# Kernel optimization log

Measured on AMD Instinct MI355X. Metric: run time of the kernel, lower is better.

## Reference

```python
import jax, jax.numpy as jnp
import numpy as np

B, C, H, W = 16, 128, 64, 64
NH = 8
HD = C // NH          # head dim == pos_embed_dim
WIN = 5               # relative-position window
OUT = 512             # out_dim of the final 1x1 projection


def _dwconv(x, w, pad):
    """Depthwise 2D conv, x: (N, Cin, H, W), w: (Cin, 1, kh, kw)."""
    return jax.lax.conv_general_dilated(
        x, w, window_strides=(1, 1), padding=[(pad, pad), (pad, pad)],
        dimension_numbers=('NCHW', 'OIHW', 'NCHW'),
        feature_group_count=x.shape[1])


def setup_inputs() -> dict:
    key = jax.random.key(0)
    ks = jax.random.split(key, 6)
    src = jax.random.normal(ks[0], (B, C, H, W), jnp.float32)
    cpe_w = jax.random.normal(ks[1], (C, 1, 3, 3), jnp.float32) * 0.1
    qkv_w = jax.random.normal(ks[2], (3 * C, C), jnp.float32) * (1.0 / np.sqrt(C))
    rel_pos = jax.random.normal(ks[3], (HD, WIN, WIN), jnp.float32) * 0.02
    conv1d_w = jax.random.normal(ks[4], (3,), jnp.float32) * 0.5
    out_w = jax.random.normal(ks[5], (OUT, 2 * C), jnp.float32) * (1.0 / np.sqrt(2 * C))
    return dict(src=src, cpe_w=cpe_w, qkv_w=qkv_w, rel_pos=rel_pos,
                conv1d_w=conv1d_w, out_w=out_w)


def reference(src, cpe_w, qkv_w, rel_pos, conv1d_w, out_w):
    scaling = HD ** (-0.5)
    feature_raw = src

    # CPE: depthwise 3x3 conv residual
    s = _dwconv(src, cpe_w, 1) + src

    # 1x1 QKV conv == channel GEMM
    qkv = jnp.einsum('oc,bchw->bohw', qkv_w, s)          # (B, 3C, H, W)
    q, k, v = jnp.split(qkv, 3, axis=1)                  # each (B, C, H, W)

    q = q.reshape(B * NH, HD, H, W)
    k = k.reshape(B * NH, HD, H, W)
    v = v.reshape(B * NH, HD, H, W)

    N = H * W
    kf = jax.nn.softmax(k.reshape(B * NH, HD, N), axis=-1)   # softmax over spatial
    vf = v.reshape(B * NH, HD, N)
    content_lambda = jnp.einsum('bin,bon->bio', kf, vf)      # (B*NH, HD, HD)
    qf = q.reshape(B * NH, HD, N) * scaling
    content_output = jnp.einsum('bin,bio->bon', qf, content_lambda)
    content_output = content_output.reshape(B * NH, HD, H, W)

    # relative-position lambda: depthwise 5x5 conv of v with rel_pos_embed
    position_lambda = _dwconv(v, rel_pos[:, None, :, :], WIN // 2)
    position_output = q * position_lambda

    result1 = (content_output + position_output).reshape(B, C, H, W)

    # ECA-style channel attention on the raw input
    pool = jnp.mean(feature_raw, axis=(2, 3))                # (B, C)
    xp = jnp.pad(pool, ((0, 0), (1, 1)))
    ca = jax.nn.sigmoid(conv1d_w[0] * xp[:, :-2]
                        + conv1d_w[1] * xp[:, 1:-1]
                        + conv1d_w[2] * xp[:, 2:])           # (B, C)
    result2 = feature_raw * ca[:, :, None, None]

    cat = jnp.concatenate([result1, result2], axis=1)       # (B, 2C, H, W)
    return jnp.einsum('oc,bchw->bohw', out_w, cat)           # (B, OUT, H, W)
```

## Files before the change

### kernel.cpp

```cpp
#include <hip/hip_runtime.h>
#include <hip/hip_bf16.h>
#include <math.h>

#define Bb   16
#define Cc   128
#define Hh   64
#define Wwid 64
#define Nn   4096
#define NHh  8
#define HDd  16
#define BHh  128
#define TCc  384
#define OUTc 512
#define KK2  256

typedef _Float16 f16x8 __attribute__((ext_vector_type(8)));
typedef float    f32x4 __attribute__((ext_vector_type(4)));

__device__ __forceinline__ ushort f2h_bits(float f) {
    _Float16 h = (_Float16)f;
    ushort u;
    __builtin_memcpy(&u, &h, 2);
    return u;
}
__device__ __forceinline__ float h2f_bits(ushort u) {
    _Float16 h;
    __builtin_memcpy(&h, &u, 2);
    return (float)h;
}

__global__ void __launch_bounds__(256) cpe_cvt_kernel(
        const float* __restrict__ src, const float* __restrict__ cpe_w,
        const float* __restrict__ qkv_w, const float* __restrict__ out_w,
        ushort* __restrict__ s, ushort* __restrict__ src16,
        float* __restrict__ pool,
        ushort* __restrict__ wq16, ushort* __restrict__ wo16) {
    int t = threadIdx.x;
    if (blockIdx.x >= 2048) {
        int i = (blockIdx.x - 2048) * 256 + t;
        const int na = TCc * Cc, nb = OUTc * KK2;
        if (i < na) wq16[i] = f2h_bits(qkv_w[i]);
        else if (i < na + nb) wo16[i - na] = f2h_bits(out_w[i - na]);
        return;
    }
    int bc = blockIdx.x;
    int c  = bc & (Cc - 1);
    const float* sp = src + (size_t)bc * Nn;
    __shared__ float pl[66 * 66];
    __shared__ float red[256];
    for (int i = t; i < 66 * 66; i += 256) pl[i] = 0.f;
    __syncthreads();
    float lsum = 0.f;
    ushort* s16p = src16 + (size_t)bc * Nn;
    for (int i = t; i < Nn / 4; i += 256) {
        float4 v4 = ((const float4*)sp)[i];
        lsum += v4.x + v4.y + v4.z + v4.w;
        ushort4 h4 = make_ushort4(f2h_bits(v4.x), f2h_bits(v4.y),
                                  f2h_bits(v4.z), f2h_bits(v4.w));
        *(ushort4*)(s16p + i * 4) = h4;
        int e = i * 4, y = e >> 6, x = e & 63;
        float* d = &pl[(y + 1) * 66 + x + 1];
        d[0] = v4.x; d[1] = v4.y; d[2] = v4.z; d[3] = v4.w;
    }
    red[t] = lsum;
    float w[9];
#pragma unroll
    for (int k = 0; k < 9; k++) w[k] = cpe_w[c * 9 + k];
    __syncthreads();
    for (int s2 = 128; s2 > 0; s2 >>= 1) {
        if (t < s2) red[t] += red[t + s2];
        __syncthreads();
    }
    if (t == 0) pool[bc] = red[0] * (1.0f / Nn);
    int x = t & 63, ys = (t >> 6) * 16;
    float r[3][3];
#pragma unroll
    for (int k = 0; k < 2; k++)
#pragma unroll
        for (int j = 0; j < 3; j++) r[k][j] = pl[(ys + k) * 66 + x + j];
    ushort* dst = s + (size_t)bc * Nn;
#pragma unroll
    for (int yy = 0; yy < 16; yy++) {
        int y = ys + yy;
#pragma unroll
        for (int j = 0; j < 3; j++) r[2][j] = pl[(y + 2) * 66 + x + j];
        float acc = r[1][1];
#pragma unroll
        for (int k = 0; k < 3; k++)
#pragma unroll
            for (int j = 0; j < 3; j++) acc += r[k][j] * w[k * 3 + j];
        dst[y * 64 + x] = f2h_bits(acc);
#pragma unroll
        for (int j = 0; j < 3; j++) { r[0][j] = r[1][j]; r[1][j] = r[2][j]; }
    }
}

__global__ void transpose_s(const ushort* __restrict__ s, ushort* __restrict__ sT) {
    int bz = blockIdx.z;
    int c0 = blockIdx.y * 64;
    int n0 = blockIdx.x * 64;
    __shared__ ushort t[64][68];
    int nn = threadIdx.x & 63, c4 = threadIdx.x >> 6;
    const ushort* sp = s + ((size_t)bz * Cc + c0) * Nn + n0;
#pragma unroll
    for (int p = 0; p < 16; p++) {
        int cc = p * 4 + c4;
        t[cc][nn] = sp[(size_t)cc * Nn + nn];
    }
    __syncthreads();
    int cw = threadIdx.x & 63, n4 = threadIdx.x >> 6;
    ushort* dp = sT + ((size_t)bz * Nn + n0) * Cc + c0;
#pragma unroll
    for (int p = 0; p < 16; p++) {
        int n = p * 4 + n4;
        dp[(size_t)n * Cc + cw] = t[cw][n];
    }
}

template<int K, int M, int MODE>
__global__ void __launch_bounds__(256) gemm_tn(const ushort* __restrict__ A,
                                               const ushort* __restrict__ Bt,
                                               float* __restrict__ C,
                                               ushort* __restrict__ q16,
                                               float* __restrict__ kf32,
                                               ushort* __restrict__ v16) {
    const int bz = blockIdx.z;
    const int m0 = blockIdx.y * 128;
    const int n0 = blockIdx.x * 128;
    __shared__ __align__(16) ushort Al[2][128 * 32];
    __shared__ __align__(16) ushort Bl[2][128 * 32];
    __shared__ __align__(16) float  ep[4][16][66];
    const int tid  = threadIdx.x;
    const int wave = tid >> 6, lane = tid & 63;
    const int r = lane & 15, q = lane >> 4;
    const int wr = wave >> 1, wc = wave & 1;

    const ushort* Ag = A + (size_t)m0 * K;
    const ushort* Bg = Bt + ((size_t)bz * Nn + n0) * K;

    f32x4 acc[4][4] = {};

    auto stage = [&](int buf, int k0) {
#pragma unroll
        for (int p = 0; p < 2; p++) {
            int seg = p * 4 + wave;
            int idx = seg * 64 + lane;
            int row = idx >> 2, ch = idx & 3;
            const ushort* ga = Ag + (size_t)row * K + k0 + ch * 8;
            const ushort* gb = Bg + (size_t)row * K + k0 + ch * 8;
            __builtin_amdgcn_global_load_lds(
                (const __attribute__((address_space(1))) void*)(const void*)ga,
                (__attribute__((address_space(3))) void*)(void*)(&Al[buf][seg * 512]),
                16, 0, 0);
            __builtin_amdgcn_global_load_lds(
                (const __attribute__((address_space(1))) void*)(const void*)gb,
                (__attribute__((address_space(3))) void*)(void*)(&Bl[buf][seg * 512]),
                16, 0, 0);
        }
    };

    constexpr int NT = K / 32;
    stage(0, 0);
    __syncthreads();
#pragma unroll
    for (int t = 0; t < NT; t++) {
        const int cur = t & 1;
        if (t + 1 < NT) stage(cur ^ 1, (t + 1) * 32);

        const ushort* Apt = &Al[cur][(wr * 64 + r) * 32 + q * 8];
        const ushort* Bpt = &Bl[cur][(wc * 64 + r) * 32 + q * 8];
        f16x8 af[4], bf[4];
#pragma unroll
        for (int i = 0; i < 4; i++) af[i] = *(const f16x8*)(Apt + i * 16 * 32);
#pragma unroll
        for (int j = 0; j < 4; j++) bf[j] = *(const f16x8*)(Bpt + j * 16 * 32);
#pragma unroll
        for (int i = 0; i < 4; i++)
#pragma unroll
            for (int j = 0; j < 4; j++)
                acc[i][j] = __builtin_amdgcn_mfma_f32_16x16x32_f16(af[i], bf[j], acc[i][j], 0, 0, 0);
        if (t + 1 < NT) __syncthreads();
    }

    if constexpr (MODE == 0) {
        float* Cp = C + ((size_t)bz * M + m0 + wr * 64) * Nn + n0 + wc * 64;
#pragma unroll
        for (int i = 0; i < 4; i++) {
#pragma unroll
            for (int j = 0; j < 4; j++)
#pragma unroll
                for (int e = 0; e < 4; e++)
                    ep[wave][q * 4 + e][j * 16 + r] = acc[i][j][e];
#pragma unroll
            for (int rep = 0; rep < 4; rep++) {
                int rl = rep * 4 + q;
                float4 v = *(const float4*)&ep[wave][rl][r * 4];
                *(float4*)&Cp[(size_t)(i * 16 + rl) * Nn + r * 4] = v;
            }
        }
    } else {
        size_t base = ((size_t)bz * Cc + wr * 64) * Nn + n0 + wc * 64;
        if (blockIdx.y == 1) {
            float* Cp = kf32 + base;
#pragma unroll
            for (int i = 0; i < 4; i++) {
#pragma unroll
                for (int j = 0; j < 4; j++)
#pragma unroll
                    for (int e = 0; e < 4; e++)
                        ep[wave][q * 4 + e][j * 16 + r] = acc[i][j][e];
#pragma unroll
                for (int rep = 0; rep < 4; rep++) {
                    int rl = rep * 4 + q;
                    float4 v = *(const float4*)&ep[wave][rl][r * 4];
                    *(float4*)&Cp[(size_t)(i * 16 + rl) * Nn + r * 4] = v;
                }
            }
        } else {
            ushort* Cp = (blockIdx.y == 0 ? q16 : v16) + base;
#pragma unroll
            for (int i = 0; i < 4; i++) {
#pragma unroll
                for (int j = 0; j < 4; j++)
#pragma unroll
                    for (int e = 0; e < 4; e++)
                        ep[wave][q * 4 + e][j * 16 + r] = acc[i][j][e];
#pragma unroll
                for (int rep = 0; rep < 4; rep++) {
                    int rl = rep * 4 + q;
                    float4 v = *(const float4*)&ep[wave][rl][r * 4];
                    uint2 pk;
                    pk.x = (uint)f2h_bits(v.x) | ((uint)f2h_bits(v.y) << 16);
                    pk.y = (uint)f2h_bits(v.z) | ((uint)f2h_bits(v.w) << 16);
                    *(uint2*)&Cp[(size_t)(i * 16 + rl) * Nn + r * 4] = pk;
                }
            }
        }
    }
}

__global__ void __launch_bounds__(256) lam_pos_kernel(
        const float* __restrict__ kf32, const ushort* __restrict__ v16,
        const float* __restrict__ rel,
        ushort* __restrict__ pos, float* __restrict__ lamP,
        float* __restrict__ lamE) {
    __shared__ float smem[68 * 68];
    int t = threadIdx.x;

    if (blockIdx.x >= 2048) {
        int bid2 = blockIdx.x - 2048;
        int bh   = bid2 >> 1;
        int half = bid2 & 1;
        int b = bh >> 3, h = bh & 7;
        int wave = t >> 6, lane = t & 63;
        int r = lane & 15, q = lane >> 4;
        const float*  kf = kf32 + ((size_t)b * Cc + h * HDd) * Nn;
        const ushort* vf = v16  + ((size_t)b * Cc + h * HDd) * Nn;

        f32x4 acc = {};
        float esum = 0.f;
        int nbase = half * 2048 + wave * 512;
#pragma unroll 4
        for (int s = 0; s < 16; s++) {
            int n = nbase + s * 32 + q * 8;
            float4 ka = *(const float4*)(kf + (size_t)r * Nn + n);
            float4 kb = *(const float4*)(kf + (size_t)r * Nn + n + 4);
            f16x8 bf = *(const f16x8*)(vf + (size_t)r * Nn + n);
            float e0 = __expf(ka.x), e1 = __expf(ka.y), e2 = __expf(ka.z), e3 = __expf(ka.w);
            float e4 = __expf(kb.x), e5 = __expf(kb.y), e6 = __expf(kb.z), e7 = __expf(kb.w);
            esum += (e0 + e1 + e2 + e3) + (e4 + e5 + e6 + e7);
            f16x8 af;
            af[0] = (_Float16)e0; af[1] = (_Float16)e1;
            af[2] = (_Float16)e2; af[3] = (_Float16)e3;
            af[4] = (_Float16)e4; af[5] = (_Float16)e5;
            af[6] = (_Float16)e6; af[7] = (_Float16)e7;
            acc = __builtin_amdgcn_mfma_f32_16x16x32_f16(af, bf, acc, 0, 0, 0);
        }

        float* red   = smem;
        float* esred = smem + 1024;
#pragma unroll
        for (int e = 0; e < 4; e++) red[wave * 256 + lane * 4 + e] = acc[e];
        esred[wave * 64 + lane] = esum;
        __syncthreads();
        if (wave == 0) {
#pragma unroll
            for (int e = 0; e < 4; e++) {
                float v = red[0 * 256 + lane * 4 + e] + red[1 * 256 + lane * 4 + e]
                        + red[2 * 256 + lane * 4 + e] + red[3 * 256 + lane * 4 + e];
                int row = q * 4 + e;
                lamP[(size_t)half * (BHh * 256) + bh * 256 + row * 16 + r] = v;
            }
            if (lane < 16) {
                float tot = 0.f;
#pragma unroll
                for (int w2 = 0; w2 < 4; w2++)
#pragma unroll
                    for (int qq = 0; qq < 4; qq++)
                        tot += esred[w2 * 64 + qq * 16 + lane];
                lamE[(size_t)half * (BHh * 16) + bh * 16 + lane] = tot;
            }
        }
        return;
    }

    int bc = blockIdx.x;
    int c = bc & (Cc - 1);
    const ushort* vp = v16 + (size_t)bc * Nn;
    float* pl = smem;
    for (int i = t; i < 68 * 68; i += 256) pl[i] = 0.f;
    __syncthreads();
    for (int i = t; i < Nn / 8; i += 256) {
        uint4 u = ((const uint4*)vp)[i];
        ushort us[8]; *(uint4*)us = u;
        int e = i * 8, y = e >> 6, x = e & 63;
        float* d = &pl[(y + 2) * 68 + x + 2];
#pragma unroll
        for (int j = 0; j < 8; j++) d[j] = h2f_bits(us[j]);
    }
    float w[25];
#pragma unroll
    for (int k = 0; k < 25; k++) w[k] = rel[(c & (HDd - 1)) * 25 + k];
    __syncthreads();
    int x = t & 63, ys = (t >> 6) * 16;
    float r[5][5];
#pragma unroll
    for (int k = 0; k < 4; k++)
#pragma unroll
        for (int j = 0; j < 5; j++) r[k][j] = pl[(ys + k) * 68 + x + j];
    ushort* dst = pos + (size_t)bc * Nn;
#pragma unroll
    for (int yy = 0; yy < 16; yy++) {
        int y = ys + yy;
#pragma unroll
        for (int j = 0; j < 5; j++) r[4][j] = pl[(y + 4) * 68 + x + j];
        float acc = 0.f;
#pragma unroll
        for (int k = 0; k < 5; k++)
#pragma unroll
            for (int j = 0; j < 5; j++) acc += r[k][j] * w[k * 5 + j];
        dst[y * 64 + x] = f2h_bits(acc);
#pragma unroll
        for (int k = 0; k < 4; k++)
#pragma unroll
            for (int j = 0; j < 5; j++) r[k][j] = r[k + 1][j];
    }
}

__global__ void __launch_bounds__(256) combine_eca_kernel(
        const ushort* __restrict__ q16, const float* __restrict__ lamP,
        const float* __restrict__ lamE, const ushort* __restrict__ pos,
        const ushort* __restrict__ src16, const float* __restrict__ pool,
        const float* __restrict__ w3, ushort* __restrict__ catT) {
    __shared__ float smem[2240];
    int tid = threadIdx.x;

    if (blockIdx.x >= 2048) {
        int bid2 = blockIdx.x - 2048;
        int n0 = (bid2 & 63) * 64, c0 = ((bid2 >> 6) & 1) * 64, bz = bid2 >> 7;
        ushort* t = (ushort*)smem;
        float* ca_s = smem + 2176;
        if (tid < 64) {
            int c = c0 + tid;
            float left  = (c == 0)        ? 0.f : pool[bz * Cc + c - 1];
            float mid   = pool[bz * Cc + c];
            float right = (c == Cc - 1)   ? 0.f : pool[bz * Cc + c + 1];
            float v = w3[0] * left + w3[1] * mid + w3[2] * right;
            ca_s[tid] = 1.f / (1.f + __expf(-v));
        }
        __syncthreads();
        int nn = tid & 63, c4 = tid >> 6;
        const ushort* sp = src16 + ((size_t)bz * Cc + c0) * Nn + n0;
#pragma unroll
        for (int p = 0; p < 16; p++) {
            int cc = p * 4 + c4;
            t[cc * 68 + nn] = f2h_bits(h2f_bits(sp[(size_t)cc * Nn + nn]) * ca_s[cc]);
        }
        __syncthreads();
        int cw = tid & 63, n4 = tid >> 6;
        ushort* dp = catT + ((size_t)bz * Nn + n0) * KK2 + Cc + c0;
#pragma unroll
        for (int p = 0; p < 16; p++) {
            int n = p * 4 + n4;
            dp[(size_t)n * KK2 + cw] = t[cw * 68 + n];
        }
        return;
    }

    int bh   = blockIdx.x >> 4;
    int tile = blockIdx.x & 15;
    int n = tile * 256 + tid;
    int b = bh >> 3, h = bh & 7;
    float* lam_s = smem;
    {
        int i = tid >> 4;
        float es = lamE[bh * 16 + i] + lamE[(size_t)(BHh * 16) + bh * 16 + i];
        lam_s[tid] = (lamP[bh * 256 + tid]
                    + lamP[(size_t)(BHh * 256) + bh * 256 + tid]) / es;
    }
    __syncthreads();
    const ushort* qp = q16 + ((size_t)b * Cc + h * HDd) * Nn;
    float qv[16];
#pragma unroll
    for (int i = 0; i < 16; i++) qv[i] = h2f_bits(qp[(size_t)i * Nn + n]);
    const ushort* pp = pos + ((size_t)b * Cc + h * HDd) * Nn;
    float vals[16];
#pragma unroll
    for (int o = 0; o < 16; o++) {
        float co = 0.f;
#pragma unroll
        for (int i2 = 0; i2 < 16; i2++) co += qv[i2] * lam_s[i2 * 16 + o];
        vals[o] = co * 0.25f + qv[o] * h2f_bits(pp[(size_t)o * Nn + n]);
    }
    uint up[8];
#pragma unroll
    for (int o2 = 0; o2 < 8; o2++)
        up[o2] = (uint)f2h_bits(vals[2 * o2]) | ((uint)f2h_bits(vals[2 * o2 + 1]) << 16);
    uint4* dst = (uint4*)(catT + ((size_t)b * Nn + n) * KK2 + h * HDd);
    dst[0] = make_uint4(up[0], up[1], up[2], up[3]);
    dst[1] = make_uint4(up[4], up[5], up[6], up[7]);
}

extern "C" void kernel_launch(void* const* d_in, const int* in_sizes, int n_in,
                              void* d_out, int out_size, void* d_ws, size_t ws_size,
                              hipStream_t stream) {
    const float* src      = (const float*)d_in[0];
    const float* cpe_w    = (const float*)d_in[1];
    const float* qkv_w    = (const float*)d_in[2];
    const float* rel_pos  = (const float*)d_in[3];
    const float* conv1d_w = (const float*)d_in[4];
    const float* out_w    = (const float*)d_in[5];
    float* out = (float*)d_out;

    char* ws = (char*)d_ws;
    ushort* q16   = (ushort*)ws;                                 ws += (size_t)Bb * Cc * Nn * 2;
    float*  kf32  = (float*)ws;                                  ws += (size_t)Bb * Cc * Nn * 4;
    ushort* v16   = (ushort*)ws;                                 ws += (size_t)Bb * Cc * Nn * 2;
    ushort* pos   = (ushort*)ws;                                 ws += (size_t)Bb * Cc * Nn * 2;
    ushort* catT  = (ushort*)ws;                                 ws += (size_t)Bb * Nn * KK2 * 2;
    ushort* sT    = (ushort*)ws;                                 ws += (size_t)Bb * Nn * Cc * 2;
    ushort* src16 = (ushort*)ws;                                 ws += (size_t)Bb * Cc * Nn * 2;
    ushort* s16   = (ushort*)catT;
    float*  lamP  = (float*)ws;                                  ws += (size_t)2 * BHh * 256 * 4;
    float*  lamE  = (float*)ws;                                  ws += (size_t)2 * BHh * 16 * 4;
    float*  pool  = (float*)ws;                                  ws += Bb * Cc * 4;
    ushort* wq16  = (ushort*)ws;                                 ws += (size_t)TCc * Cc * 2;
    ushort* wo16  = (ushort*)ws;                                 ws += (size_t)OUTc * KK2 * 2;

    {
        const int nw = TCc * Cc + OUTc * KK2;
        int cvt_blocks = (nw + 255) / 256;
        cpe_cvt_kernel<<<2048 + cvt_blocks, 256, 0, stream>>>(
            src, cpe_w, qkv_w, out_w, s16, src16, pool, wq16, wo16);
    }
    {
        dim3 g(Nn / 64, Cc / 64, Bb);
        transpose_s<<<g, 256, 0, stream>>>(s16, sT);
    }
    {
        dim3 g(Nn / 128, TCc / 128, Bb);
        gemm_tn<Cc, TCc, 1><<<g, 256, 0, stream>>>(wq16, sT, nullptr, q16, kf32, v16);
    }
    lam_pos_kernel<<<2048 + 2 * BHh, 256, 0, stream>>>(kf32, v16, rel_pos, pos, lamP, lamE);
    combine_eca_kernel<<<2048 + 2048, 256, 0, stream>>>(
        q16, lamP, lamE, pos, src16, pool, conv1d_w, catT);
    {
        dim3 g(Nn / 128, OUTc / 128, Bb);
        gemm_tn<KK2, OUTc, 0><<<g, 256, 0, stream>>>(wo16, catT, out, nullptr, nullptr, nullptr);
    }
}
```

Measured before the change: 260.0 us.

## Template GEMM on M-waves, use 256-row tiles for output projection

Parameterizes the GEMM on the number of wave rows, so the output projection uses 256x128 tiles with 512 threads while the QKV GEMM keeps its 128x128 configuration. The larger tile reuses each staged B (activation) tile across twice as many output rows, halving B global reads for the final projection. Shared memory is unioned between the staging buffers and the epilogue scratch, which needs an extra barrier. Output stores become nontemporal. The larger block uses more LDS and registers per block, which may reduce occupancy and leaves fewer blocks in the grid.

```diff
diff --git a/kernel.cpp b/kernel.cpp
--- a/kernel.cpp
+++ b/kernel.cpp
@@ -117,19 +117,27 @@
     }
 }
 
-template<int K, int M, int MODE>
-__global__ void __launch_bounds__(256) gemm_tn(const ushort* __restrict__ A,
-                                               const ushort* __restrict__ Bt,
-                                               float* __restrict__ C,
-                                               ushort* __restrict__ q16,
-                                               float* __restrict__ kf32,
-                                               ushort* __restrict__ v16) {
+template<int K, int M, int MODE, int WM>
+__global__ void __launch_bounds__(WM * 128) gemm_tn(const ushort* __restrict__ A,
+                                                    const ushort* __restrict__ Bt,
+                                                    float* __restrict__ C,
+                                                    ushort* __restrict__ q16,
+                                                    float* __restrict__ kf32,
+                                                    ushort* __restrict__ v16) {
+    constexpr int BM   = WM * 64;
+    constexpr int NW   = WM * 2;
+    constexpr int ABUF = BM * 32;
+    constexpr int BBUF = 128 * 32;
+    constexpr size_t BUF_BYTES = (size_t)(2 * ABUF + 2 * BBUF) * 2;
+    constexpr size_t EP_BYTES  = (size_t)NW * 16 * 66 * 4;
+    constexpr size_t SMEM_BYTES = BUF_BYTES > EP_BYTES ? BUF_BYTES : EP_BYTES;
+    __shared__ __align__(16) char smem[SMEM_BYTES];
+    ushort* Abase = (ushort*)smem;
+    ushort* Bbase = Abase + 2 * ABUF;
+
     const int bz = blockIdx.z;
-    const int m0 = blockIdx.y * 128;
+    const int m0 = blockIdx.y * BM;
     const int n0 = blockIdx.x * 128;
-    __shared__ __align__(16) ushort Al[2][128 * 32];
-    __shared__ __align__(16) ushort Bl[2][128 * 32];
-    __shared__ __align__(16) float  ep[4][16][66];
     const int tid  = threadIdx.x;
     const int wave = tid >> 6, lane = tid & 63;
     const int r = lane & 15, q = lane >> 4;
@@ -141,20 +149,26 @@
     f32x4 acc[4][4] = {};
 
     auto stage = [&](int buf, int k0) {
+        ushort* Ad = Abase + buf * ABUF;
+        ushort* Bd = Bbase + buf * BBUF;
 #pragma unroll
         for (int p = 0; p < 2; p++) {
-            int seg = p * 4 + wave;
+            int seg = p * NW + wave;
             int idx = seg * 64 + lane;
             int row = idx >> 2, ch = idx & 3;
-            const ushort* ga = Ag + (size_t)row * K + k0 + ch * 8;
-            const ushort* gb = Bg + (size_t)row * K + k0 + ch * 8;
             __builtin_amdgcn_global_load_lds(
-                (const __attribute__((address_space(1))) void*)(const void*)ga,
-                (__attribute__((address_space(3))) void*)(void*)(&Al[buf][seg * 512]),
+                (const __attribute__((address_space(1))) void*)(const void*)(Ag + (size_t)row * K + k0 + ch * 8),
+                (__attribute__((address_space(3))) void*)(void*)(Ad + seg * 512),
                 16, 0, 0);
+        }
+#pragma unroll
+        for (int p = 0; p < 8 / NW; p++) {
+            int seg = p * NW + wave;
+            int idx = seg * 64 + lane;
+            int row = idx >> 2, ch = idx & 3;
             __builtin_amdgcn_global_load_lds(
-                (const __attribute__((address_space(1))) void*)(const void*)gb,
-                (__attribute__((address_space(3))) void*)(void*)(&Bl[buf][seg * 512]),
+                (const __attribute__((address_space(1))) void*)(const void*)(Bg + (size_t)row * K + k0 + ch * 8),
+                (__attribute__((address_space(3))) void*)(void*)(Bd + seg * 512),
                 16, 0, 0);
         }
     };
@@ -167,8 +181,8 @@
         const int cur = t & 1;
         if (t + 1 < NT) stage(cur ^ 1, (t + 1) * 32);
 
-        const ushort* Apt = &Al[cur][(wr * 64 + r) * 32 + q * 8];
-        const ushort* Bpt = &Bl[cur][(wc * 64 + r) * 32 + q * 8];
+        const ushort* Apt = Abase + cur * ABUF + (wr * 64 + r) * 32 + q * 8;
+        const ushort* Bpt = Bbase + cur * BBUF + (wc * 64 + r) * 32 + q * 8;
         f16x8 af[4], bf[4];
 #pragma unroll
         for (int i = 0; i < 4; i++) af[i] = *(const f16x8*)(Apt + i * 16 * 32);
@@ -182,6 +196,9 @@
         if (t + 1 < NT) __syncthreads();
     }
 
+    __syncthreads();
+    float (*ep)[16][66] = (float (*)[16][66])smem;
+
     if constexpr (MODE == 0) {
         float* Cp = C + ((size_t)bz * M + m0 + wr * 64) * Nn + n0 + wc * 64;
 #pragma unroll
@@ -194,8 +211,8 @@
 #pragma unroll
             for (int rep = 0; rep < 4; rep++) {
                 int rl = rep * 4 + q;
-                float4 v = *(const float4*)&ep[wave][rl][r * 4];
-                *(float4*)&Cp[(size_t)(i * 16 + rl) * Nn + r * 4] = v;
+                f32x4 v = *(const f32x4*)&ep[wave][rl][r * 4];
+                __builtin_nontemporal_store(v, (f32x4*)&Cp[(size_t)(i * 16 + rl) * Nn + r * 4]);
             }
         }
     } else {
@@ -459,13 +476,13 @@
     }
     {
         dim3 g(Nn / 128, TCc / 128, Bb);
-        gemm_tn<Cc, TCc, 1><<<g, 256, 0, stream>>>(wq16, sT, nullptr, q16, kf32, v16);
+        gemm_tn<Cc, TCc, 1, 2><<<g, 256, 0, stream>>>(wq16, sT, nullptr, q16, kf32, v16);
     }
     lam_pos_kernel<<<2048 + 2 * BHh, 256, 0, stream>>>(kf32, v16, rel_pos, pos, lamP, lamE);
     combine_eca_kernel<<<2048 + 2048, 256, 0, stream>>>(
         q16, lamP, lamE, pos, src16, pool, conv1d_w, catT);
     {
-        dim3 g(Nn / 128, OUTc / 128, Bb);
-        gemm_tn<KK2, OUTc, 0><<<g, 256, 0, stream>>>(wo16, catT, out, nullptr, nullptr, nullptr);
-    }
-}
+        dim3 g(Nn / 128, OUTc / 256, Bb);
+        gemm_tn<KK2, OUTc, 0, 4><<<g, 512, 0, stream>>>(wo16, catT, out, nullptr, nullptr, nullptr);
+    }
+}
```

Measured after the change: 257.5 us. Within noise of the previous version (-0.9%).
